# Performance work log

Measured on AMD Instinct MI355X. Metric: run time of the kernel, lower is better.

## Reference

```python
import jax, jax.numpy as jnp
import numpy as np

B, T, C = 256, 2048, 39   # batch, time, nb_filters
NB = 8                     # number of dilation levels (2**0 .. 2**7)
K = 2                      # kernel size
NC = 8                     # num_classes
EPS = 1e-5                 # BatchNorm eps (eval mode)


def _causal_conv(x, w, b, d):
    """x: [B,C,T], w: [Cout,Cin,K], left-pad (K-1)*d for causality."""
    k = w.shape[-1]
    y = jax.lax.conv_general_dilated(
        x, w, window_strides=(1,), padding=[((k - 1) * d, 0)],
        rhs_dilation=(d,), dimension_numbers=('NCH', 'OIH', 'NCH'))
    return y + b[None, :, None]


def _bn(x, g, be, m, v):
    # eval-mode BatchNorm1d with running stats
    return g[None, :, None] * (x - m[None, :, None]) * jax.lax.rsqrt(v + EPS)[None, :, None] + be[None, :, None]


def _block(x, w, b, g, be, m, v, d):
    # Temporal_Aware_Block, eval mode (dropout = identity).
    # w: [2,C,C,K], b/g/be/m/v: [2,C]
    y = jax.nn.relu(_bn(_causal_conv(x, w[0], b[0], d), g[0], be[0], m[0], v[0]))
    y = jax.nn.relu(_bn(_causal_conv(y, w[1], b[1], d), g[1], be[1], m[1], v[1]))
    # causal conv preserves length, so the 1x1 residual conv branch is never taken
    return x * jax.nn.sigmoid(y)


def setup_inputs() -> dict:
    key = jax.random.key(0)
    ks = jax.random.split(key, 24)
    f = lambda k, s: jax.random.normal(k, s, dtype=jnp.float32) * 0.1
    return {
        'inputs': jax.random.normal(ks[0], (B, T, C), dtype=jnp.float32),
        'conv1x1_w': f(ks[1], (C, C, 1)),
        'conv1x1_b': f(ks[2], (C,)),
        'fw_conv_w': f(ks[3], (NB, 2, C, C, K)),
        'fw_conv_b': f(ks[4], (NB, 2, C)),
        'fw_gamma': 1.0 + f(ks[5], (NB, 2, C)),
        'fw_beta': f(ks[6], (NB, 2, C)),
        'fw_mean': f(ks[7], (NB, 2, C)),
        'fw_var': jax.random.uniform(ks[8], (NB, 2, C), dtype=jnp.float32, minval=0.5, maxval=1.5),
        'bw_conv_w': f(ks[9], (NB, 2, C, C, K)),
        'bw_conv_b': f(ks[10], (NB, 2, C)),
        'bw_gamma': 1.0 + f(ks[11], (NB, 2, C)),
        'bw_beta': f(ks[12], (NB, 2, C)),
        'bw_mean': f(ks[13], (NB, 2, C)),
        'bw_var': jax.random.uniform(ks[14], (NB, 2, C), dtype=jnp.float32, minval=0.5, maxval=1.5),
        'wl_kernel': f(ks[15], (NB, 1)),
        'cls_w': f(ks[16], (NC, C)),
        'cls_b': f(ks[17], (NC,)),
    }


def reference(inputs, conv1x1_w, conv1x1_b,
              fw_conv_w, fw_conv_b, fw_gamma, fw_beta, fw_mean, fw_var,
              bw_conv_w, bw_conv_b, bw_gamma, bw_beta, bw_mean, bw_var,
              wl_kernel, cls_w, cls_b):
    x = jnp.transpose(inputs, (0, 2, 1))           # [B,C,T]
    fwd = _causal_conv(x, conv1x1_w, conv1x1_b, 1)
    bwd = _causal_conv(x[:, :, ::-1], conv1x1_w, conv1x1_b, 1)
    skips = []
    for i in range(NB):
        d = 2 ** i
        fwd = _block(fwd, fw_conv_w[i], fw_conv_b[i], fw_gamma[i], fw_beta[i], fw_mean[i], fw_var[i], d)
        bwd = _block(bwd, bw_conv_w[i], bw_conv_b[i], bw_gamma[i], bw_beta[i], bw_mean[i], bw_var[i], d)
        skips.append(jnp.mean(fwd + bwd, axis=-1))  # [B,C]
    g = jnp.stack(skips, axis=-1)                   # [B,C,NB]
    x2 = jnp.einsum('bcn,no->bc', g, wl_kernel)     # WeightLayer matmul + squeeze
    logits = x2 @ cls_w.T + cls_b                   # [B,NC]
    return jax.nn.log_softmax(logits, axis=1)
```

## Files before the change

### kernel.cpp

```cpp
#include <hip/hip_runtime.h>
#include <math.h>

#define BATCH 256
#define TT    2048
#define CC    39
#define CP    40
#define Y1ST  44
#define NBLK  8
#define KK    2
#define NCLS  8
#define BN_EPS 1e-5f
#define TBLK  512
#define NW    8

typedef __attribute__((ext_vector_type(8))) short short8;
typedef __attribute__((ext_vector_type(4))) float floatx4;

__device__ __forceinline__ unsigned short f2b(float f) {
    union { float f; unsigned u; } v; v.f = f;
    unsigned r = v.u + 0x7FFF + ((v.u >> 16) & 1);
    return (unsigned short)(r >> 16);
}
__device__ __forceinline__ unsigned cvtpk(float lo, float hi) {
    unsigned r;
    asm("v_cvt_pk_bf16_f32 %0, %1, %2" : "=v"(r) : "v"(lo), "v"(hi));
    return r;
}
__device__ __forceinline__ float blo(unsigned u) {
    union { unsigned v; float f; } k; k.v = u << 16; return k.f;
}
__device__ __forceinline__ float bhi(unsigned u) {
    union { unsigned v; float f; } k; k.v = u & 0xffff0000u; return k.f;
}
__device__ __forceinline__ void gl_lds16(const void* g, void* l) {
    __builtin_amdgcn_global_load_lds(
        (const __attribute__((address_space(1))) unsigned int*)g,
        (__attribute__((address_space(3))) unsigned int*)l, 16, 0, 0);
}

#define WFB_PER   (2*3*3*512)
#define WFB_TOTAL (2*NBLK*WFB_PER)
#define BFB_TOTAL (2*NBLK*2*48)
#define WFF_TOTAL (3*2*512)
#define BFF_TOTAL 48
#define ZPAD_SHORTS (256 * CP)

__global__ void fold_kernel(const float* __restrict__ fw_w, const float* __restrict__ fw_b,
                            const float* __restrict__ fw_g, const float* __restrict__ fw_be,
                            const float* __restrict__ fw_m, const float* __restrict__ fw_v,
                            const float* __restrict__ bw_w, const float* __restrict__ bw_b,
                            const float* __restrict__ bw_g, const float* __restrict__ bw_be,
                            const float* __restrict__ bw_m, const float* __restrict__ bw_v,
                            const float* __restrict__ c1w, const float* __restrict__ c1b,
                            unsigned short* __restrict__ wfb, float* __restrict__ bfb,
                            unsigned short* __restrict__ wff, float* __restrict__ bff) {
    int idx = blockIdx.x * blockDim.x + threadIdx.x;
    if (idx < WFB_TOTAL) {
        int i = idx;
        int reg = i & 7;   i >>= 3;
        int lane = i & 63; i >>= 6;
        int sl = i % 3;    i /= 3;
        int ct = i % 3;    i /= 3;
        int layer = i & 1; i >>= 1;
        int blk = i & 7;   i >>= 3;
        int dir = i;
        int g = lane >> 4;
        int co = ct * 16 + (lane & 15);
        int p, ci; bool ok = true;
        if (sl < 2) {
            int kin = (g << 3) + reg;
            p = kin >> 4;
            ci = sl * 16 + (kin & 15);
        } else {
            p = g & 1;
            ci = 32 + reg;
            ok = (g < 2);
        }
        float val = 0.f;
        if (ok && co < CC && ci < CC) {
            const float* w = dir ? bw_w : fw_w;
            const float* gam = dir ? bw_g : fw_g;
            const float* var = dir ? bw_v : fw_v;
            int il = blk * 2 + layer;
            float sc = gam[il * CC + co] * rsqrtf(var[il * CC + co] + BN_EPS);
            val = w[((size_t)(il * CC + co) * CC + ci) * KK + p] * sc;
        }
        wfb[idx] = f2b(val);
        return;
    }
    idx -= WFB_TOTAL;
    if (idx < BFB_TOTAL) {
        int co = idx % 48;
        int i = idx / 48;
        int layer = i & 1; i >>= 1;
        int blk = i & 7;   i >>= 3;
        int dir = i;
        float val = 0.f;
        if (co < CC) {
            const float* b  = dir ? bw_b  : fw_b;
            const float* g  = dir ? bw_g  : fw_g;
            const float* be = dir ? bw_be : fw_be;
            const float* m  = dir ? bw_m  : fw_m;
            const float* v  = dir ? bw_v  : fw_v;
            int r = (blk * 2 + layer) * CC + co;
            float sc = g[r] * rsqrtf(v[r] + BN_EPS);
            val = (b[r] - m[r]) * sc + be[r];
        }
        bfb[idx] = val;
        return;
    }
    idx -= BFB_TOTAL;
    if (idx < WFF_TOTAL) {
        int i = idx;
        int reg = i & 7;   i >>= 3;
        int lane = i & 63; i >>= 6;
        int sl = i & 1;    i >>= 1;
        int ct = i;
        int co = ct * 16 + (lane & 15);
        int ci = sl * 32 + ((lane >> 4) << 3) + reg;
        float val = (co < CC && ci < CC) ? c1w[co * CC + ci] : 0.f;
        wff[idx] = f2b(val);
        return;
    }
    idx -= WFF_TOTAL;
    if (idx < BFF_TOTAL) {
        bff[idx] = (idx < CC) ? c1b[idx] : 0.f;
    }
}

__global__ __launch_bounds__(TBLK) void block0_mfma(
        const float* __restrict__ in,
        const unsigned short* __restrict__ wf_all, const float* __restrict__ bf_all,
        const unsigned short* __restrict__ wff, const float* __restrict__ bff,
        unsigned short* __restrict__ yg, float* __restrict__ skipPart) {
    constexpr int D = 1;
    constexpr int ROWS_X   = 272;
    constexpr int XT_SHORTS = ROWS_X * CP;
    constexpr int M1       = 17;
    constexpr int ROWS_REAL = 256 + D;
    constexpr int Y1_SHORTS = M1 * 16 * Y1ST + 8;
    constexpr int M2W      = 256 / (16 * NW);

    extern __shared__ char ldsraw[];
    unsigned short* xt = (unsigned short*)ldsraw;
    unsigned short* y1 = xt + XT_SHORTS;
    float* stash = (float*)(y1 + Y1_SHORTS);

    const int dir = blockIdx.z, b = blockIdx.y, tile = blockIdx.x;
    const int t0 = tile * 256;
    const int tid = threadIdx.x, lane = tid & 63, wave = tid >> 6;
    const int c = lane & 15, g = lane >> 4;
    const size_t cbase = (size_t)(dir * BATCH + b) * TT * CP;

    {
        unsigned* xd = (unsigned*)xt;
        const float* inb = in + (size_t)b * TT * CC;
        for (int e = tid; e < ROWS_X * 20; e += TBLK) {
            int row = e / 20, cp = e - row * 20;
            int t = t0 - 2 + row;
            unsigned val = 0u;
            if (t >= 0 && row < 258) {
                int srow = dir ? (TT - 1 - t) : t;
                const float* sp = inb + (size_t)srow * CC + cp * 2;
                float f0 = sp[0];
                float f1 = (cp < 19) ? sp[1] : 0.f;
                val = cvtpk(f0, f1);
            }
            xd[e] = val;
        }
        if (tid < 16) ((unsigned*)(xt + XT_SHORTS))[tid] = 0;
    }

    short8 FW[3][2];
    float fbs[3][4];
#pragma unroll
    for (int ct = 0; ct < 3; ++ct) {
#pragma unroll
        for (int sl = 0; sl < 2; ++sl)
            FW[ct][sl] = *(const short8*)(wff + (((ct * 2 + sl) * 64 + lane) << 3));
#pragma unroll
        for (int j = 0; j < 4; ++j) fbs[ct][j] = bff[ct * 16 + g * 4 + j];
    }
    __syncthreads();

    for (int mt = wave; mt < M1; mt += NW) {
        int row = (mt << 4) + c;
        const unsigned short* bp = xt + row * CP;
        floatx4 acc[3];
#pragma unroll
        for (int ct = 0; ct < 3; ++ct)
            acc[ct] = floatx4{fbs[ct][0], fbs[ct][1], fbs[ct][2], fbs[ct][3]};
#pragma unroll
        for (int sl = 0; sl < 2; ++sl) {
            short8 B = *(const short8*)(bp + sl * 32 + g * 8);
#pragma unroll
            for (int ct = 0; ct < 3; ++ct)
                acc[ct] = __builtin_amdgcn_mfma_f32_16x16x32_bf16(FW[ct][sl], B, acc[ct], 0, 0, 0);
        }
        unsigned short* op = xt + row * CP;
#pragma unroll
        for (int ct = 0; ct < 3; ++ct) {
            if (ct == 2 && g >= 2) continue;
            uint2 v;
            v.x = cvtpk(acc[ct][0], acc[ct][1]);
            v.y = cvtpk(acc[ct][2], acc[ct][3]);
            *(uint2*)(op + ct * 16 + g * 4) = v;
        }
    }
    __syncthreads();

    const int r01off = (g >> 1) * D;
    const int r2off  = (g & 1) * D;
    const int koff8  = (g & 1) << 3;
    const unsigned short* wf = wf_all + (size_t)(dir * NBLK + 0) * WFB_PER;
    const float* bf = bf_all + (size_t)(dir * NBLK + 0) * 96;

    short8 Wf[3][3];
    float bs[3][4];
#pragma unroll
    for (int ct = 0; ct < 3; ++ct) {
#pragma unroll
        for (int sl = 0; sl < 3; ++sl)
            Wf[ct][sl] = *(const short8*)(wf + (((ct * 3 + sl) * 64 + lane) << 3));
#pragma unroll
        for (int j = 0; j < 4; ++j) bs[ct][j] = bf[ct * 16 + g * 4 + j];
    }

    for (int mt = wave; mt < M1; mt += NW) {
        int j0 = mt << 4;
        const unsigned short* bp01 = xt + (j0 + c + r01off) * CP + koff8;
        const unsigned short* bp2  = xt + (j0 + c + r2off) * CP + 32;
        short8 B0 = *(const short8*)(bp01);
        short8 B1 = *(const short8*)(bp01 + 16);
        short8 B2 = *(const short8*)(bp2);
        floatx4 acc[3];
#pragma unroll
        for (int ct = 0; ct < 3; ++ct) {
            acc[ct] = floatx4{bs[ct][0], bs[ct][1], bs[ct][2], bs[ct][3]};
            acc[ct] = __builtin_amdgcn_mfma_f32_16x16x32_bf16(Wf[ct][0], B0, acc[ct], 0, 0, 0);
            acc[ct] = __builtin_amdgcn_mfma_f32_16x16x32_bf16(Wf[ct][1], B1, acc[ct], 0, 0, 0);
            acc[ct] = __builtin_amdgcn_mfma_f32_16x16x32_bf16(Wf[ct][2], B2, acc[ct], 0, 0, 0);
        }
        int r = j0 + c;
        bool dead = (t0 - D + r < 0) || (r >= ROWS_REAL);
        unsigned short* yp = y1 + r * Y1ST;
#pragma unroll
        for (int ct = 0; ct < 3; ++ct) {
            if (ct == 2 && g >= 2) continue;
            uint2 v;
            v.x = cvtpk(fmaxf(acc[ct][0], 0.f), fmaxf(acc[ct][1], 0.f));
            v.y = cvtpk(fmaxf(acc[ct][2], 0.f), fmaxf(acc[ct][3], 0.f));
            if (dead) { v.x = 0u; v.y = 0u; }
            *(uint2*)(yp + ct * 16 + g * 4) = v;
        }
    }
    __syncthreads();

#pragma unroll
    for (int ct = 0; ct < 3; ++ct) {
#pragma unroll
        for (int sl = 0; sl < 3; ++sl)
            Wf[ct][sl] = *(const short8*)(wf + ((((3 + ct) * 3 + sl) * 64 + lane) << 3));
#pragma unroll
        for (int j = 0; j < 4; ++j) bs[ct][j] = bf[48 + ct * 16 + g * 4 + j];
    }

    float sums[3][4];
#pragma unroll
    for (int ct = 0; ct < 3; ++ct)
#pragma unroll
        for (int j = 0; j < 4; ++j) sums[ct][j] = 0.f;

#pragma unroll
    for (int mi = 0; mi < M2W; ++mi) {
        int j0 = (((wave * M2W) + mi) << 4);
        const unsigned short* bp01 = y1 + (j0 + c + r01off) * Y1ST + koff8;
        const unsigned short* bp2  = y1 + (j0 + c + r2off) * Y1ST + 32;
        short8 B0 = *(const short8*)(bp01);
        short8 B1 = *(const short8*)(bp01 + 16);
        short8 B2 = *(const short8*)(bp2);
        floatx4 acc[3];
#pragma unroll
        for (int ct = 0; ct < 3; ++ct) {
            acc[ct] = floatx4{bs[ct][0], bs[ct][1], bs[ct][2], bs[ct][3]};
            acc[ct] = __builtin_amdgcn_mfma_f32_16x16x32_bf16(Wf[ct][0], B0, acc[ct], 0, 0, 0);
            acc[ct] = __builtin_amdgcn_mfma_f32_16x16x32_bf16(Wf[ct][1], B1, acc[ct], 0, 0, 0);
            acc[ct] = __builtin_amdgcn_mfma_f32_16x16x32_bf16(Wf[ct][2], B2, acc[ct], 0, 0, 0);
        }
        int r = j0 + c;
        const unsigned short* xrow = xt + (r + 2 * D) * CP;
        unsigned short* orow = yg + cbase + (size_t)(t0 + r) * CP;
#pragma unroll
        for (int ct = 0; ct < 3; ++ct) {
            uint2 xv = *(const uint2*)(xrow + ct * 16 + g * 4);
            float g0 = blo(xv.x) * __builtin_amdgcn_rcpf(1.f + __expf(-acc[ct][0]));
            float g1 = bhi(xv.x) * __builtin_amdgcn_rcpf(1.f + __expf(-acc[ct][1]));
            float g2 = blo(xv.y) * __builtin_amdgcn_rcpf(1.f + __expf(-acc[ct][2]));
            float g3 = bhi(xv.y) * __builtin_amdgcn_rcpf(1.f + __expf(-acc[ct][3]));
            sums[ct][0] += g0; sums[ct][1] += g1;
            sums[ct][2] += g2; sums[ct][3] += g3;
            if (!(ct == 2 && g >= 2)) {
                uint2 v;
                v.x = cvtpk(g0, g1);
                v.y = cvtpk(g2, g3);
                *(uint2*)(orow + ct * 16 + g * 4) = v;
            }
        }
    }
#pragma unroll
    for (int ct = 0; ct < 3; ++ct)
#pragma unroll
        for (int j = 0; j < 4; ++j) {
            float v = sums[ct][j];
            v += __shfl_xor(v, 1, 64);
            v += __shfl_xor(v, 2, 64);
            v += __shfl_xor(v, 4, 64);
            v += __shfl_xor(v, 8, 64);
            sums[ct][j] = v;
        }
    if (c == 0) {
#pragma unroll
        for (int ct = 0; ct < 3; ++ct)
#pragma unroll
            for (int j = 0; j < 4; ++j)
                stash[wave * 48 + ct * 16 + g * 4 + j] = sums[ct][j];
    }
    __syncthreads();
    if (tid < CC) {
        float s = 0.f;
#pragma unroll
        for (int w = 0; w < NW; ++w) s += stash[w * 48 + tid];
        skipPart[(((size_t)(0 * 2 + dir) * BATCH + b) * CC + tid) * 16 + tile] = s;
    }
}

template <int D, int TtC>
__global__ __launch_bounds__(TBLK) void block_mfma(const unsigned short* __restrict__ xg,
                                                   unsigned short* __restrict__ yg,
                                                   const unsigned short* __restrict__ wf_all,
                                                   const float* __restrict__ bf_all,
                                                   float* __restrict__ skipPart,
                                                   const unsigned short* __restrict__ zpad,
                                                   int blk, int writeOut) {
    constexpr int NW_      = TBLK / 64;
    constexpr int ROWS_X   = TtC + 2 * D;
    constexpr int NCH      = ROWS_X * 5;
    constexpr int NIT      = (NCH + TBLK - 1) / TBLK;
    constexpr int XT_SHORTS = ROWS_X * CP;
    constexpr int M1       = (TtC + D + 15) / 16;
    constexpr int ROWS_REAL = TtC + D;
    constexpr int Y1_SHORTS = M1 * 16 * Y1ST + 8;
    constexpr int M2W      = TtC / (16 * NW_);

    extern __shared__ char ldsraw[];
    unsigned short* xt = (unsigned short*)ldsraw;
    unsigned short* y1 = xt + XT_SHORTS;
    float* stash = (float*)(y1 + Y1_SHORTS);

    const int dir = blockIdx.z, b = blockIdx.y, tile = blockIdx.x;
    const int t0 = tile * TtC;
    const int tid = threadIdx.x, lane = tid & 63, wave = tid >> 6;
    const int c = lane & 15, g = lane >> 4;

    const size_t cbase = (size_t)(dir * BATCH + b) * TT * CP;
    const unsigned short* wf = wf_all + (size_t)(dir * NBLK + blk) * WFB_PER;
    const float* bf = bf_all + (size_t)(dir * NBLK + blk) * 96;

    {
        const unsigned short* gx = xg + cbase;
#pragma unroll
        for (int it = 0; it < NIT; ++it) {
            int chunk = it * TBLK + wave * 64 + lane;
            if (chunk < NCH) {
                unsigned row = (unsigned)chunk / 5u;
                int sub = chunk - (int)row * 5;
                int t = t0 - 2 * D + (int)row;
                const unsigned short* src = (t >= 0)
                    ? (gx + (size_t)t * CP + sub * 8)
                    : (zpad + (row * CP + sub * 8));
                gl_lds16(src, xt + (size_t)(it * TBLK + wave * 64) * 8);
            }
        }
    }

    short8 Wf[3][3];
#pragma unroll
    for (int ct = 0; ct < 3; ++ct)
#pragma unroll
        for (int sl = 0; sl < 3; ++sl)
            Wf[ct][sl] = *(const short8*)(wf + ((((0 * 3 + ct) * 3 + sl) * 64 + lane) << 3));
    float bs[3][4];
#pragma unroll
    for (int ct = 0; ct < 3; ++ct)
#pragma unroll
        for (int j = 0; j < 4; ++j) bs[ct][j] = bf[ct * 16 + g * 4 + j];

    __syncthreads();

    const int r01off = (g >> 1) * D;
    const int r2off  = (g & 1) * D;
    const int koff8  = (g & 1) << 3;

    for (int mt = wave; mt < M1; mt += NW_) {
        int j0 = mt << 4;
        const unsigned short* bp01 = xt + (j0 + c + r01off) * CP + koff8;
        const unsigned short* bp2  = xt + (j0 + c + r2off) * CP + 32;
        short8 B0 = *(const short8*)(bp01);
        short8 B1 = *(const short8*)(bp01 + 16);
        short8 B2 = *(const short8*)(bp2);
        floatx4 acc[3];
#pragma unroll
        for (int ct = 0; ct < 3; ++ct) {
            acc[ct] = floatx4{bs[ct][0], bs[ct][1], bs[ct][2], bs[ct][3]};
            acc[ct] = __builtin_amdgcn_mfma_f32_16x16x32_bf16(Wf[ct][0], B0, acc[ct], 0, 0, 0);
            acc[ct] = __builtin_amdgcn_mfma_f32_16x16x32_bf16(Wf[ct][1], B1, acc[ct], 0, 0, 0);
            acc[ct] = __builtin_amdgcn_mfma_f32_16x16x32_bf16(Wf[ct][2], B2, acc[ct], 0, 0, 0);
        }
        int r = j0 + c;
        bool dead = (t0 - D + r < 0) || (r >= ROWS_REAL);
        unsigned short* yp = y1 + r * Y1ST;
#pragma unroll
        for (int ct = 0; ct < 3; ++ct) {
            if (ct == 2 && g >= 2) continue;
            uint2 v;
            v.x = cvtpk(fmaxf(acc[ct][0], 0.f), fmaxf(acc[ct][1], 0.f));
            v.y = cvtpk(fmaxf(acc[ct][2], 0.f), fmaxf(acc[ct][3], 0.f));
            if (dead) { v.x = 0u; v.y = 0u; }
            *(uint2*)(yp + ct * 16 + g * 4) = v;
        }
    }
    __syncthreads();

#pragma unroll
    for (int ct = 0; ct < 3; ++ct)
#pragma unroll
        for (int sl = 0; sl < 3; ++sl)
            Wf[ct][sl] = *(const short8*)(wf + ((((1 * 3 + ct) * 3 + sl) * 64 + lane) << 3));
#pragma unroll
    for (int ct = 0; ct < 3; ++ct)
#pragma unroll
        for (int j = 0; j < 4; ++j) bs[ct][j] = bf[48 + ct * 16 + g * 4 + j];

    float sums[3][4];
#pragma unroll
    for (int ct = 0; ct < 3; ++ct)
#pragma unroll
        for (int j = 0; j < 4; ++j) sums[ct][j] = 0.f;

#pragma unroll
    for (int mi = 0; mi < M2W; ++mi) {
        int j0 = (wave * M2W + mi) << 4;
        const unsigned short* bp01 = y1 + (j0 + c + r01off) * Y1ST + koff8;
        const unsigned short* bp2  = y1 + (j0 + c + r2off) * Y1ST + 32;
        short8 B0 = *(const short8*)(bp01);
        short8 B1 = *(const short8*)(bp01 + 16);
        short8 B2 = *(const short8*)(bp2);
        floatx4 acc[3];
#pragma unroll
        for (int ct = 0; ct < 3; ++ct) {
            acc[ct] = floatx4{bs[ct][0], bs[ct][1], bs[ct][2], bs[ct][3]};
            acc[ct] = __builtin_amdgcn_mfma_f32_16x16x32_bf16(Wf[ct][0], B0, acc[ct], 0, 0, 0);
            acc[ct] = __builtin_amdgcn_mfma_f32_16x16x32_bf16(Wf[ct][1], B1, acc[ct], 0, 0, 0);
            acc[ct] = __builtin_amdgcn_mfma_f32_16x16x32_bf16(Wf[ct][2], B2, acc[ct], 0, 0, 0);
        }
        int r = j0 + c;
        const unsigned short* xrow = xt + (r + 2 * D) * CP;
        unsigned short* orow = yg + cbase + (size_t)(t0 + r) * CP;
#pragma unroll
        for (int ct = 0; ct < 3; ++ct) {
            uint2 xv = *(const uint2*)(xrow + ct * 16 + g * 4);
            float g0 = blo(xv.x) * __builtin_amdgcn_rcpf(1.f + __expf(-acc[ct][0]));
            float g1 = bhi(xv.x) * __builtin_amdgcn_rcpf(1.f + __expf(-acc[ct][1]));
            float g2 = blo(xv.y) * __builtin_amdgcn_rcpf(1.f + __expf(-acc[ct][2]));
            float g3 = bhi(xv.y) * __builtin_amdgcn_rcpf(1.f + __expf(-acc[ct][3]));
            sums[ct][0] += g0; sums[ct][1] += g1;
            sums[ct][2] += g2; sums[ct][3] += g3;
            if (writeOut && !(ct == 2 && g >= 2)) {
                uint2 v;
                v.x = cvtpk(g0, g1);
                v.y = cvtpk(g2, g3);
                *(uint2*)(orow + ct * 16 + g * 4) = v;
            }
        }
    }
#pragma unroll
    for (int ct = 0; ct < 3; ++ct)
#pragma unroll
        for (int j = 0; j < 4; ++j) {
            float v = sums[ct][j];
            v += __shfl_xor(v, 1, 64);
            v += __shfl_xor(v, 2, 64);
            v += __shfl_xor(v, 4, 64);
            v += __shfl_xor(v, 8, 64);
            sums[ct][j] = v;
        }
    if (c == 0) {
#pragma unroll
        for (int ct = 0; ct < 3; ++ct)
#pragma unroll
            for (int j = 0; j < 4; ++j)
                stash[wave * 48 + ct * 16 + g * 4 + j] = sums[ct][j];
    }
    __syncthreads();
    if (tid < CC) {
        float s = 0.f;
#pragma unroll
        for (int w = 0; w < NW_; ++w) s += stash[w * 48 + tid];
        skipPart[(((size_t)(blk * 2 + dir) * BATCH + b) * CC + tid) * 16 + tile] = s;
    }
}

static inline size_t lds_bytes_for(int D, int Tt) {
    int rows_x = Tt + 2 * D;
    int xt_shorts = rows_x * CP;
    int m1 = (Tt + D + 15) / 16;
    int y1_shorts = m1 * 16 * Y1ST + 8;
    return (size_t)(xt_shorts + y1_shorts) * 2 + (TBLK / 64) * 48 * 4;
}

__global__ __launch_bounds__(64) void tail_kernel(const float* __restrict__ skipPart,
                                                  const float* __restrict__ wl,
                                                  const float* __restrict__ cw,
                                                  const float* __restrict__ cb,
                                                  float* __restrict__ out) {
    __shared__ float xs[CC];
    int b = blockIdx.x;
    int cth = threadIdx.x;
    if (cth < CC) {
        float x2 = 0.f;
        for (int i = 0; i < NBLK; ++i) {
            float wli = wl[i] * (1.0f / TT);
            for (int dirn = 0; dirn < 2; ++dirn) {
                const float* sp = skipPart + (((size_t)(i * 2 + dirn) * BATCH + b) * CC + cth) * 16;
                float s = 0.f;
#pragma unroll
                for (int tl = 0; tl < 8; ++tl) s += sp[tl];
                x2 = fmaf(s, wli, x2);
            }
        }
        xs[cth] = x2;
    }
    __syncthreads();
    if (threadIdx.x == 0) {
        float lg[NCLS];
        float mx = -1e30f;
        for (int o = 0; o < NCLS; ++o) {
            float a = cb[o];
#pragma unroll
            for (int cc2 = 0; cc2 < CC; ++cc2) a = fmaf(cw[o * CC + cc2], xs[cc2], a);
            lg[o] = a;
            mx = fmaxf(mx, a);
        }
        float se = 0.f;
        for (int o = 0; o < NCLS; ++o) se += expf(lg[o] - mx);
        float lse = logf(se) + mx;
        for (int o = 0; o < NCLS; ++o) out[b * NCLS + o] = lg[o] - lse;
    }
}

extern "C" void kernel_launch(void* const* d_in, const int* in_sizes, int n_in,
                              void* d_out, int out_size, void* d_ws, size_t ws_size,
                              hipStream_t stream) {
    const float* inputs = (const float*)d_in[0];
    const float* c1w    = (const float*)d_in[1];
    const float* c1b    = (const float*)d_in[2];
    const float* fw_w   = (const float*)d_in[3];
    const float* fw_b   = (const float*)d_in[4];
    const float* fw_g   = (const float*)d_in[5];
    const float* fw_be  = (const float*)d_in[6];
    const float* fw_m   = (const float*)d_in[7];
    const float* fw_v   = (const float*)d_in[8];
    const float* bw_w   = (const float*)d_in[9];
    const float* bw_b   = (const float*)d_in[10];
    const float* bw_g   = (const float*)d_in[11];
    const float* bw_be  = (const float*)d_in[12];
    const float* bw_m   = (const float*)d_in[13];
    const float* bw_v   = (const float*)d_in[14];
    const float* wl     = (const float*)d_in[15];
    const float* clsw   = (const float*)d_in[16];
    const float* clsb   = (const float*)d_in[17];

    const size_t bufsz = (size_t)2 * BATCH * TT * CP;
    unsigned short* buf0 = (unsigned short*)d_ws;
    unsigned short* buf1 = buf0 + bufsz;
    float* skip = (float*)(buf1 + bufsz);
    const size_t skipsz = (size_t)NBLK * 2 * BATCH * CC * 16;
    unsigned short* wfb = (unsigned short*)(skip + skipsz);
    float* bfb = (float*)(wfb + WFB_TOTAL);
    unsigned short* wff = (unsigned short*)(bfb + BFB_TOTAL);
    float* bff = (float*)(wff + WFF_TOTAL);
    unsigned short* zpad = (unsigned short*)(bff + BFF_TOTAL);

    hipMemsetAsync(zpad, 0, ZPAD_SHORTS * sizeof(unsigned short), stream);

    {
        int tot = WFB_TOTAL + BFB_TOTAL + WFF_TOTAL + BFF_TOTAL;
        fold_kernel<<<(tot + 255) / 256, 256, 0, stream>>>(
            fw_w, fw_b, fw_g, fw_be, fw_m, fw_v,
            bw_w, bw_b, bw_g, bw_be, bw_m, bw_v, c1w, c1b,
            wfb, bfb, wff, bff);
    }

    {
        size_t lds0 = (size_t)(272 * CP + 17 * 16 * Y1ST + 8) * 2 + (TBLK / 64) * 48 * 4 + 64;
        block0_mfma<<<dim3(TT / 256, BATCH, 2), TBLK, lds0, stream>>>(
            inputs, wfb, bfb, wff, bff, buf0, skip);
    }

    unsigned short* cur = buf0;
    unsigned short* nxt = buf1;
#define LAUNCH_BLOCK(DD)                                                             \
    block_mfma<DD, 256><<<dim3(TT / 256, BATCH, 2), TBLK, lds_bytes_for(DD, 256),    \
                          stream>>>(cur, nxt, wfb, bfb, skip, zpad, i,               \
                                    (i < NBLK - 1) ? 1 : 0)
    for (int i = 1; i < NBLK; ++i) {
        switch (i) {
            case 1: LAUNCH_BLOCK(2); break;
            case 2: LAUNCH_BLOCK(4); break;
            case 3: LAUNCH_BLOCK(8); break;
            case 4: LAUNCH_BLOCK(16); break;
            case 5: LAUNCH_BLOCK(32); break;
            case 6: LAUNCH_BLOCK(64); break;
            case 7: LAUNCH_BLOCK(128); break;
        }
        unsigned short* tmp = cur; cur = nxt; nxt = tmp;
    }
#undef LAUNCH_BLOCK

    tail_kernel<<<BATCH, 64, 0, stream>>>(skip, wl, clsw, clsb, (float*)d_out);
}
```

Baseline: 558.3 us.

## Fuse pairs of low-dilation temporal blocks into one kernel with halo recompute

Adds a pair_mfma kernel that runs two consecutive dilated blocks (levels 1-2 and 3-4) in one launch. The first block's output for the tile plus the halo the second block needs is kept in LDS, so the intermediate activation never goes through global memory. Fused launches use 128-step tiles, so there are now 16 skip partials per tile; the tail sums all 16 and the skip buffer is zeroed. The cost is recomputing halo rows and more LDS per block.

```diff
diff --git a/kernel.cpp b/kernel.cpp
--- a/kernel.cpp
+++ b/kernel.cpp
@@ -334,6 +334,315 @@
     }
 }
 
+template <int DA, int DB, int LA, int TtC>
+__global__ __launch_bounds__(TBLK) void pair_mfma(
+        const unsigned short* __restrict__ xg, unsigned short* __restrict__ yg,
+        const unsigned short* __restrict__ wf_all, const float* __restrict__ bf_all,
+        float* __restrict__ skipPart, const unsigned short* __restrict__ zpad) {
+    constexpr int HX  = 2 * DB + 2 * DA;
+    constexpr int HYA = 2 * DB + DA;
+    constexpr int RXR = TtC + HX;
+    constexpr int RYA = TtC + HYA;
+    constexpr int M1A = (RYA + 15) / 16;
+    constexpr int RXA = M1A * 16 + DA;
+    constexpr int RYB = TtC + DB;
+    constexpr int M1B = (RYB + 15) / 16;
+    constexpr int RAR = TtC + 2 * DB;
+    constexpr int RAA = ((M1B * 16 + DB + 15) / 16) * 16;
+    constexpr int M2A = RAA / 16;
+    constexpr int M2B = TtC / (16 * NW);
+    constexpr int XSH  = RXA * CP;
+    constexpr int Y1SH = M1A * 16 * Y1ST + 8;
+    constexpr int ASH  = RAA * CP;
+    constexpr int NCHA = RXA * 5;
+    constexpr int NIT  = (NCHA + TBLK - 1) / TBLK;
+    constexpr int NTIL = TT / TtC;
+
+    extern __shared__ char ldsraw[];
+    unsigned short* X  = (unsigned short*)ldsraw;
+    unsigned short* Y1 = X + XSH;
+    unsigned short* AO = Y1 + Y1SH;
+    float* stash = (float*)(AO + ASH);
+
+    const int dir = blockIdx.z, b = blockIdx.y, tile = blockIdx.x;
+    const int t0 = tile * TtC;
+    const int tid = threadIdx.x, lane = tid & 63, wave = tid >> 6;
+    const int c = lane & 15, g = lane >> 4;
+    const int koff8 = (g & 1) << 3;
+    const int oa01 = (g >> 1) * DA, oa2 = (g & 1) * DA;
+    const int ob01 = (g >> 1) * DB, ob2 = (g & 1) * DB;
+
+    const size_t cbase = (size_t)(dir * BATCH + b) * TT * CP;
+    const unsigned short* wfa = wf_all + (size_t)(dir * NBLK + LA) * WFB_PER;
+    const float* bfa = bf_all + (size_t)(dir * NBLK + LA) * 96;
+    const unsigned short* wfb2 = wf_all + (size_t)(dir * NBLK + LA + 1) * WFB_PER;
+    const float* bfb2 = bf_all + (size_t)(dir * NBLK + LA + 1) * 96;
+
+    {
+        const unsigned short* gx = xg + cbase;
+#pragma unroll
+        for (int it = 0; it < NIT; ++it) {
+            int chunk = it * TBLK + wave * 64 + lane;
+            if (chunk < NCHA) {
+                unsigned row = (unsigned)chunk / 5u;
+                int sub = chunk - (int)row * 5;
+                int t = t0 - HX + (int)row;
+                const unsigned short* src = (t >= 0 && (int)row < RXR)
+                    ? (gx + (size_t)t * CP + sub * 8)
+                    : (zpad + ((row & 255u) * CP + sub * 8));
+                gl_lds16(src, X + (size_t)(it * TBLK + wave * 64) * 8);
+            }
+        }
+    }
+
+    short8 Wf[3][3];
+    float bs[3][4];
+#pragma unroll
+    for (int ct = 0; ct < 3; ++ct) {
+#pragma unroll
+        for (int sl = 0; sl < 3; ++sl)
+            Wf[ct][sl] = *(const short8*)(wfa + (((ct * 3 + sl) * 64 + lane) << 3));
+#pragma unroll
+        for (int j = 0; j < 4; ++j) bs[ct][j] = bfa[ct * 16 + g * 4 + j];
+    }
+    __syncthreads();
+
+    for (int mt = wave; mt < M1A; mt += NW) {
+        int j0 = mt << 4;
+        const unsigned short* bp01 = X + (j0 + c + oa01) * CP + koff8;
+        const unsigned short* bp2  = X + (j0 + c + oa2) * CP + 32;
+        short8 B0 = *(const short8*)(bp01);
+        short8 B1 = *(const short8*)(bp01 + 16);
+        short8 B2 = *(const short8*)(bp2);
+        floatx4 acc[3];
+#pragma unroll
+        for (int ct = 0; ct < 3; ++ct) {
+            acc[ct] = floatx4{bs[ct][0], bs[ct][1], bs[ct][2], bs[ct][3]};
+            acc[ct] = __builtin_amdgcn_mfma_f32_16x16x32_bf16(Wf[ct][0], B0, acc[ct], 0, 0, 0);
+            acc[ct] = __builtin_amdgcn_mfma_f32_16x16x32_bf16(Wf[ct][1], B1, acc[ct], 0, 0, 0);
+            acc[ct] = __builtin_amdgcn_mfma_f32_16x16x32_bf16(Wf[ct][2], B2, acc[ct], 0, 0, 0);
+        }
+        int r = j0 + c;
+        bool dead = (t0 - HYA + r < 0) || (r >= RYA);
+        unsigned short* yp = Y1 + r * Y1ST;
+#pragma unroll
+        for (int ct = 0; ct < 3; ++ct) {
+            if (ct == 2 && g >= 2) continue;
+            uint2 v;
+            v.x = cvtpk(fmaxf(acc[ct][0], 0.f), fmaxf(acc[ct][1], 0.f));
+            v.y = cvtpk(fmaxf(acc[ct][2], 0.f), fmaxf(acc[ct][3], 0.f));
+            if (dead) { v.x = 0u; v.y = 0u; }
+            *(uint2*)(yp + ct * 16 + g * 4) = v;
+        }
+    }
+    __syncthreads();
+
+#pragma unroll
+    for (int ct = 0; ct < 3; ++ct) {
+#pragma unroll
+        for (int sl = 0; sl < 3; ++sl)
+            Wf[ct][sl] = *(const short8*)(wfa + ((((3 + ct) * 3 + sl) * 64 + lane) << 3));
+#pragma unroll
+        for (int j = 0; j < 4; ++j) bs[ct][j] = bfa[48 + ct * 16 + g * 4 + j];
+    }
+
+    float sums[3][4];
+#pragma unroll
+    for (int ct = 0; ct < 3; ++ct)
+#pragma unroll
+        for (int j = 0; j < 4; ++j) sums[ct][j] = 0.f;
+
+    for (int mt = wave; mt < M2A; mt += NW) {
+        int j0 = mt << 4;
+        const unsigned short* bp01 = Y1 + (j0 + c + oa01) * Y1ST + koff8;
+        const unsigned short* bp2  = Y1 + (j0 + c + oa2) * Y1ST + 32;
+        short8 B0 = *(const short8*)(bp01);
+        short8 B1 = *(const short8*)(bp01 + 16);
+        short8 B2 = *(const short8*)(bp2);
+        floatx4 acc[3];
+#pragma unroll
+        for (int ct = 0; ct < 3; ++ct) {
+            acc[ct] = floatx4{bs[ct][0], bs[ct][1], bs[ct][2], bs[ct][3]};
+            acc[ct] = __builtin_amdgcn_mfma_f32_16x16x32_bf16(Wf[ct][0], B0, acc[ct], 0, 0, 0);
+            acc[ct] = __builtin_amdgcn_mfma_f32_16x16x32_bf16(Wf[ct][1], B1, acc[ct], 0, 0, 0);
+            acc[ct] = __builtin_amdgcn_mfma_f32_16x16x32_bf16(Wf[ct][2], B2, acc[ct], 0, 0, 0);
+        }
+        int ra = j0 + c;
+        bool adead = (ra >= RAR);
+        bool inskip = (ra >= 2 * DB) && (ra < 2 * DB + TtC);
+        const unsigned short* xrow = X + (ra + 2 * DA) * CP;
+        unsigned short* arow = AO + ra * CP;
+#pragma unroll
+        for (int ct = 0; ct < 3; ++ct) {
+            if (ct == 2 && g >= 2) continue;
+            uint2 ov;
+            if (adead) {
+                ov.x = 0u; ov.y = 0u;
+            } else {
+                uint2 xv = *(const uint2*)(xrow + ct * 16 + g * 4);
+                float g0 = blo(xv.x) * __builtin_amdgcn_rcpf(1.f + __expf(-acc[ct][0]));
+                float g1 = bhi(xv.x) * __builtin_amdgcn_rcpf(1.f + __expf(-acc[ct][1]));
+                float g2 = blo(xv.y) * __builtin_amdgcn_rcpf(1.f + __expf(-acc[ct][2]));
+                float g3 = bhi(xv.y) * __builtin_amdgcn_rcpf(1.f + __expf(-acc[ct][3]));
+                if (inskip) {
+                    sums[ct][0] += g0; sums[ct][1] += g1;
+                    sums[ct][2] += g2; sums[ct][3] += g3;
+                }
+                ov.x = cvtpk(g0, g1);
+                ov.y = cvtpk(g2, g3);
+            }
+            *(uint2*)(arow + ct * 16 + g * 4) = ov;
+        }
+    }
+#pragma unroll
+    for (int ct = 0; ct < 3; ++ct)
+#pragma unroll
+        for (int j = 0; j < 4; ++j) {
+            float v = sums[ct][j];
+            v += __shfl_xor(v, 1, 64);
+            v += __shfl_xor(v, 2, 64);
+            v += __shfl_xor(v, 4, 64);
+            v += __shfl_xor(v, 8, 64);
+            sums[ct][j] = v;
+        }
+    if (c == 0) {
+#pragma unroll
+        for (int ct = 0; ct < 3; ++ct)
+#pragma unroll
+            for (int j = 0; j < 4; ++j)
+                stash[wave * 48 + ct * 16 + g * 4 + j] = sums[ct][j];
+    }
+    __syncthreads();
+    if (tid < CC) {
+        float s = 0.f;
+#pragma unroll
+        for (int w = 0; w < NW; ++w) s += stash[w * 48 + tid];
+        skipPart[(((size_t)(LA * 2 + dir) * BATCH + b) * CC + tid) * 16 + tile] = s;
+    }
+
+#pragma unroll
+    for (int ct = 0; ct < 3; ++ct) {
+#pragma unroll
+        for (int sl = 0; sl < 3; ++sl)
+            Wf[ct][sl] = *(const short8*)(wfb2 + (((ct * 3 + sl) * 64 + lane) << 3));
+#pragma unroll
+        for (int j = 0; j < 4; ++j) bs[ct][j] = bfb2[ct * 16 + g * 4 + j];
+    }
+    for (int mt = wave; mt < M1B; mt += NW) {
+        int j0 = mt << 4;
+        const unsigned short* bp01 = AO + (j0 + c + ob01) * CP + koff8;
+        const unsigned short* bp2  = AO + (j0 + c + ob2) * CP + 32;
+        short8 B0 = *(const short8*)(bp01);
+        short8 B1 = *(const short8*)(bp01 + 16);
+        short8 B2 = *(const short8*)(bp2);
+        floatx4 acc[3];
+#pragma unroll
+        for (int ct = 0; ct < 3; ++ct) {
+            acc[ct] = floatx4{bs[ct][0], bs[ct][1], bs[ct][2], bs[ct][3]};
+            acc[ct] = __builtin_amdgcn_mfma_f32_16x16x32_bf16(Wf[ct][0], B0, acc[ct], 0, 0, 0);
+            acc[ct] = __builtin_amdgcn_mfma_f32_16x16x32_bf16(Wf[ct][1], B1, acc[ct], 0, 0, 0);
+            acc[ct] = __builtin_amdgcn_mfma_f32_16x16x32_bf16(Wf[ct][2], B2, acc[ct], 0, 0, 0);
+        }
+        int r = j0 + c;
+        bool dead = (t0 - DB + r < 0) || (r >= RYB);
+        unsigned short* yp = Y1 + r * Y1ST;
+#pragma unroll
+        for (int ct = 0; ct < 3; ++ct) {
+            if (ct == 2 && g >= 2) continue;
+            uint2 v;
+            v.x = cvtpk(fmaxf(acc[ct][0], 0.f), fmaxf(acc[ct][1], 0.f));
+            v.y = cvtpk(fmaxf(acc[ct][2], 0.f), fmaxf(acc[ct][3], 0.f));
+            if (dead) { v.x = 0u; v.y = 0u; }
+            *(uint2*)(yp + ct * 16 + g * 4) = v;
+        }
+    }
+    __syncthreads();
+
+#pragma unroll
+    for (int ct = 0; ct < 3; ++ct) {
+#pragma unroll
+        for (int sl = 0; sl < 3; ++sl)
+            Wf[ct][sl] = *(const short8*)(wfb2 + ((((3 + ct) * 3 + sl) * 64 + lane) << 3));
+#pragma unroll
+        for (int j = 0; j < 4; ++j) bs[ct][j] = bfb2[48 + ct * 16 + g * 4 + j];
+    }
+#pragma unroll
+    for (int ct = 0; ct < 3; ++ct)
+#pragma unroll
+        for (int j = 0; j < 4; ++j) sums[ct][j] = 0.f;
+
+#pragma unroll
+    for (int mi = 0; mi < M2B; ++mi) {
+        int j0 = (wave * M2B + mi) << 4;
+        const unsigned short* bp01 = Y1 + (j0 + c + ob01) * Y1ST + koff8;
+        const unsigned short* bp2  = Y1 + (j0 + c + ob2) * Y1ST + 32;
+        short8 B0 = *(const short8*)(bp01);
+        short8 B1 = *(const short8*)(bp01 + 16);
+        short8 B2 = *(const short8*)(bp2);
+        floatx4 acc[3];
+#pragma unroll
+        for (int ct = 0; ct < 3; ++ct) {
+            acc[ct] = floatx4{bs[ct][0], bs[ct][1], bs[ct][2], bs[ct][3]};
+            acc[ct] = __builtin_amdgcn_mfma_f32_16x16x32_bf16(Wf[ct][0], B0, acc[ct], 0, 0, 0);
+            acc[ct] = __builtin_amdgcn_mfma_f32_16x16x32_bf16(Wf[ct][1], B1, acc[ct], 0, 0, 0);
+            acc[ct] = __builtin_amdgcn_mfma_f32_16x16x32_bf16(Wf[ct][2], B2, acc[ct], 0, 0, 0);
+        }
+        int rb = j0 + c;
+        const unsigned short* arow = AO + (rb + 2 * DB) * CP;
+        unsigned short* orow = yg + cbase + (size_t)(t0 + rb) * CP;
+#pragma unroll
+        for (int ct = 0; ct < 3; ++ct) {
+            uint2 xv = *(const uint2*)(arow + ct * 16 + g * 4);
+            float g0 = blo(xv.x) * __builtin_amdgcn_rcpf(1.f + __expf(-acc[ct][0]));
+            float g1 = bhi(xv.x) * __builtin_amdgcn_rcpf(1.f + __expf(-acc[ct][1]));
+            float g2 = blo(xv.y) * __builtin_amdgcn_rcpf(1.f + __expf(-acc[ct][2]));
+            float g3 = bhi(xv.y) * __builtin_amdgcn_rcpf(1.f + __expf(-acc[ct][3]));
+            sums[ct][0] += g0; sums[ct][1] += g1;
+            sums[ct][2] += g2; sums[ct][3] += g3;
+            if (!(ct == 2 && g >= 2)) {
+                uint2 v;
+                v.x = cvtpk(g0, g1);
+                v.y = cvtpk(g2, g3);
+                *(uint2*)(orow + ct * 16 + g * 4) = v;
+            }
+        }
+    }
+#pragma unroll
+    for (int ct = 0; ct < 3; ++ct)
+#pragma unroll
+        for (int j = 0; j < 4; ++j) {
+            float v = sums[ct][j];
+            v += __shfl_xor(v, 1, 64);
+            v += __shfl_xor(v, 2, 64);
+            v += __shfl_xor(v, 4, 64);
+            v += __shfl_xor(v, 8, 64);
+            sums[ct][j] = v;
+        }
+    if (c == 0) {
+#pragma unroll
+        for (int ct = 0; ct < 3; ++ct)
+#pragma unroll
+            for (int j = 0; j < 4; ++j)
+                stash[wave * 48 + ct * 16 + g * 4 + j] = sums[ct][j];
+    }
+    __syncthreads();
+    if (tid < CC) {
+        float s = 0.f;
+#pragma unroll
+        for (int w = 0; w < NW; ++w) s += stash[w * 48 + tid];
+        skipPart[(((size_t)((LA + 1) * 2 + dir) * BATCH + b) * CC + tid) * 16 + tile] = s;
+    }
+}
+
+static inline size_t pair_lds(int DA, int DB, int T) {
+    int HYA = 2 * DB + DA;
+    int M1A = (T + HYA + 15) / 16;
+    int RXA = M1A * 16 + DA;
+    int M1B = (T + DB + 15) / 16;
+    int RAA = ((M1B * 16 + DB + 15) / 16) * 16;
+    return (size_t)(RXA * CP + M1A * 16 * Y1ST + 8 + RAA * CP) * 2 + NW * 48 * 4;
+}
+
 template <int D, int TtC>
 __global__ __launch_bounds__(TBLK) void block_mfma(const unsigned short* __restrict__ xg,
                                                    unsigned short* __restrict__ yg,
@@ -534,7 +843,7 @@
                 const float* sp = skipPart + (((size_t)(i * 2 + dirn) * BATCH + b) * CC + cth) * 16;
                 float s = 0.f;
 #pragma unroll
-                for (int tl = 0; tl < 8; ++tl) s += sp[tl];
+                for (int tl = 0; tl < 16; ++tl) s += sp[tl];
                 x2 = fmaf(s, wli, x2);
             }
         }
@@ -592,6 +901,7 @@
     unsigned short* zpad = (unsigned short*)(bff + BFF_TOTAL);
 
     hipMemsetAsync(zpad, 0, ZPAD_SHORTS * sizeof(unsigned short), stream);
+    hipMemsetAsync(skip, 0, skipsz * sizeof(float), stream);
 
     {
         int tot = WFB_TOTAL + BFB_TOTAL + WFF_TOTAL + BFF_TOTAL;
@@ -607,25 +917,17 @@
             inputs, wfb, bfb, wff, bff, buf0, skip);
     }
 
-    unsigned short* cur = buf0;
-    unsigned short* nxt = buf1;
-#define LAUNCH_BLOCK(DD)                                                             \
-    block_mfma<DD, 256><<<dim3(TT / 256, BATCH, 2), TBLK, lds_bytes_for(DD, 256),    \
-                          stream>>>(cur, nxt, wfb, bfb, skip, zpad, i,               \
-                                    (i < NBLK - 1) ? 1 : 0)
-    for (int i = 1; i < NBLK; ++i) {
-        switch (i) {
-            case 1: LAUNCH_BLOCK(2); break;
-            case 2: LAUNCH_BLOCK(4); break;
-            case 3: LAUNCH_BLOCK(8); break;
-            case 4: LAUNCH_BLOCK(16); break;
-            case 5: LAUNCH_BLOCK(32); break;
-            case 6: LAUNCH_BLOCK(64); break;
-            case 7: LAUNCH_BLOCK(128); break;
-        }
-        unsigned short* tmp = cur; cur = nxt; nxt = tmp;
-    }
-#undef LAUNCH_BLOCK
+    pair_mfma<2, 4, 1, 128><<<dim3(TT / 128, BATCH, 2), TBLK, pair_lds(2, 4, 128), stream>>>(
+        buf0, buf1, wfb, bfb, skip, zpad);
+    pair_mfma<8, 16, 3, 128><<<dim3(TT / 128, BATCH, 2), TBLK, pair_lds(8, 16, 128), stream>>>(
+        buf1, buf0, wfb, bfb, skip, zpad);
+
+    block_mfma<32, 256><<<dim3(TT / 256, BATCH, 2), TBLK, lds_bytes_for(32, 256), stream>>>(
+        buf0, buf1, wfb, bfb, skip, zpad, 5, 1);
+    block_mfma<64, 256><<<dim3(TT / 256, BATCH, 2), TBLK, lds_bytes_for(64, 256), stream>>>(
+        buf1, buf0, wfb, bfb, skip, zpad, 6, 1);
+    block_mfma<128, 256><<<dim3(TT / 256, BATCH, 2), TBLK, lds_bytes_for(128, 256), stream>>>(
+        buf0, buf1, wfb, bfb, skip, zpad, 7, 0);
 
     tail_kernel<<<BATCH, 64, 0, stream>>>(skip, wl, clsw, clsb, (float*)d_out);
 }
```

Result: slower. 667.9 us (+19.6%).

## Process two time tiles per block with prefetched LDS double buffer for small dilations

Applied to the files above, without the earlier changes.

Adds a block2_mfma kernel for dilations 2–16. Each workgroup issues async global-to-LDS loads for two consecutive 256-step time tiles up front, then computes the first tile while the second tile's load is still in flight. This halves the grid for those levels and overlaps load latency with MFMA compute, at the cost of roughly double the LDS per block, which may reduce occupancy. Skip partial sums now use 16 slots, the skip buffer is zeroed with a memset, and the tail kernel sums all 16 slots.

```diff
diff --git a/kernel.cpp b/kernel.cpp
--- a/kernel.cpp
+++ b/kernel.cpp
@@ -334,6 +334,229 @@
     }
 }
 
+template <int D, int M1, int ROWS_REAL>
+__device__ __forceinline__ void conv1_tile(
+        const unsigned short* __restrict__ xt, unsigned short* __restrict__ y1,
+        const unsigned short* __restrict__ wf, const float* __restrict__ bf,
+        int t0, int wave, int lane) {
+    const int c = lane & 15, g = lane >> 4;
+    const int koff8 = (g & 1) << 3;
+    const int r01off = (g >> 1) * D;
+    const int r2off  = (g & 1) * D;
+    short8 Wf[3][3]; float bs[3][4];
+#pragma unroll
+    for (int ct = 0; ct < 3; ++ct) {
+#pragma unroll
+        for (int sl = 0; sl < 3; ++sl)
+            Wf[ct][sl] = *(const short8*)(wf + (((ct * 3 + sl) * 64 + lane) << 3));
+#pragma unroll
+        for (int j = 0; j < 4; ++j) bs[ct][j] = bf[ct * 16 + g * 4 + j];
+    }
+    for (int mt = wave; mt < M1; mt += NW) {
+        int j0 = mt << 4;
+        const unsigned short* bp01 = xt + (j0 + c + r01off) * CP + koff8;
+        const unsigned short* bp2  = xt + (j0 + c + r2off) * CP + 32;
+        short8 B0 = *(const short8*)(bp01);
+        short8 B1 = *(const short8*)(bp01 + 16);
+        short8 B2 = *(const short8*)(bp2);
+        floatx4 acc[3];
+#pragma unroll
+        for (int ct = 0; ct < 3; ++ct) {
+            acc[ct] = floatx4{bs[ct][0], bs[ct][1], bs[ct][2], bs[ct][3]};
+            acc[ct] = __builtin_amdgcn_mfma_f32_16x16x32_bf16(Wf[ct][0], B0, acc[ct], 0, 0, 0);
+            acc[ct] = __builtin_amdgcn_mfma_f32_16x16x32_bf16(Wf[ct][1], B1, acc[ct], 0, 0, 0);
+            acc[ct] = __builtin_amdgcn_mfma_f32_16x16x32_bf16(Wf[ct][2], B2, acc[ct], 0, 0, 0);
+        }
+        int r = j0 + c;
+        bool dead = (t0 - D + r < 0) || (r >= ROWS_REAL);
+        unsigned short* yp = y1 + r * 40;
+#pragma unroll
+        for (int ct = 0; ct < 3; ++ct) {
+            if (ct == 2 && g >= 2) continue;
+            uint2 v;
+            v.x = cvtpk(fmaxf(acc[ct][0], 0.f), fmaxf(acc[ct][1], 0.f));
+            v.y = cvtpk(fmaxf(acc[ct][2], 0.f), fmaxf(acc[ct][3], 0.f));
+            if (dead) { v.x = 0u; v.y = 0u; }
+            *(uint2*)(yp + ct * 16 + g * 4) = v;
+        }
+    }
+}
+
+template <int D, int M2W>
+__device__ __forceinline__ void conv2_tile(
+        const unsigned short* __restrict__ xt, const unsigned short* __restrict__ y1,
+        const unsigned short* __restrict__ wf, const float* __restrict__ bf,
+        unsigned short* __restrict__ ygb, int t0, int wave, int lane,
+        int writeOut, float (&sums)[3][4]) {
+    const int c = lane & 15, g = lane >> 4;
+    const int koff8 = (g & 1) << 3;
+    const int r01off = (g >> 1) * D;
+    const int r2off  = (g & 1) * D;
+    short8 Wf[3][3]; float bs[3][4];
+#pragma unroll
+    for (int ct = 0; ct < 3; ++ct) {
+#pragma unroll
+        for (int sl = 0; sl < 3; ++sl)
+            Wf[ct][sl] = *(const short8*)(wf + ((((3 + ct) * 3 + sl) * 64 + lane) << 3));
+#pragma unroll
+        for (int j = 0; j < 4; ++j) bs[ct][j] = bf[48 + ct * 16 + g * 4 + j];
+    }
+#pragma unroll
+    for (int mi = 0; mi < M2W; ++mi) {
+        int j0 = (wave * M2W + mi) << 4;
+        const unsigned short* bp01 = y1 + (j0 + c + r01off) * 40 + koff8;
+        const unsigned short* bp2  = y1 + (j0 + c + r2off) * 40 + 32;
+        short8 B0 = *(const short8*)(bp01);
+        short8 B1 = *(const short8*)(bp01 + 16);
+        short8 B2 = *(const short8*)(bp2);
+        floatx4 acc[3];
+#pragma unroll
+        for (int ct = 0; ct < 3; ++ct) {
+            acc[ct] = floatx4{bs[ct][0], bs[ct][1], bs[ct][2], bs[ct][3]};
+            acc[ct] = __builtin_amdgcn_mfma_f32_16x16x32_bf16(Wf[ct][0], B0, acc[ct], 0, 0, 0);
+            acc[ct] = __builtin_amdgcn_mfma_f32_16x16x32_bf16(Wf[ct][1], B1, acc[ct], 0, 0, 0);
+            acc[ct] = __builtin_amdgcn_mfma_f32_16x16x32_bf16(Wf[ct][2], B2, acc[ct], 0, 0, 0);
+        }
+        int r = j0 + c;
+        const unsigned short* xrow = xt + (r + 2 * D) * CP;
+        unsigned short* orow = ygb + (size_t)(t0 + r) * CP;
+#pragma unroll
+        for (int ct = 0; ct < 3; ++ct) {
+            uint2 xv = *(const uint2*)(xrow + ct * 16 + g * 4);
+            float g0 = blo(xv.x) * __builtin_amdgcn_rcpf(1.f + __expf(-acc[ct][0]));
+            float g1 = bhi(xv.x) * __builtin_amdgcn_rcpf(1.f + __expf(-acc[ct][1]));
+            float g2 = blo(xv.y) * __builtin_amdgcn_rcpf(1.f + __expf(-acc[ct][2]));
+            float g3 = bhi(xv.y) * __builtin_amdgcn_rcpf(1.f + __expf(-acc[ct][3]));
+            sums[ct][0] += g0; sums[ct][1] += g1;
+            sums[ct][2] += g2; sums[ct][3] += g3;
+            if (writeOut && !(ct == 2 && g >= 2)) {
+                uint2 v;
+                v.x = cvtpk(g0, g1);
+                v.y = cvtpk(g2, g3);
+                *(uint2*)(orow + ct * 16 + g * 4) = v;
+            }
+        }
+    }
+}
+
+template <int D>
+__global__ __launch_bounds__(TBLK) void block2_mfma(
+        const unsigned short* __restrict__ xg, unsigned short* __restrict__ yg,
+        const unsigned short* __restrict__ wf_all, const float* __restrict__ bf_all,
+        float* __restrict__ skipPart, const unsigned short* __restrict__ zpad,
+        int blk, int writeOut) {
+    constexpr int T = 256;
+    constexpr int ROWS_X = T + 2 * D;
+    constexpr int NCH = ROWS_X * 5;
+    constexpr int NIT = (NCH + TBLK - 1) / TBLK;
+    static_assert(NIT == 3, "vmcnt literal assumes NIT==3 (D<=16)");
+    constexpr int XT_CH = NIT * TBLK;
+    constexpr int XT_SHORTS = XT_CH * 8;
+    constexpr int M1 = (T + D + 15) / 16;
+    constexpr int ROWS_REAL = T + D;
+    constexpr int Y1_SHORTS = M1 * 16 * 40 + 8;
+    constexpr int M2W = T / (16 * NW);
+
+    extern __shared__ char ldsraw[];
+    unsigned short* xtA = (unsigned short*)ldsraw;
+    unsigned short* xtB = xtA + XT_SHORTS;
+    unsigned short* y1  = xtB + XT_SHORTS;
+    float* stash = (float*)(y1 + Y1_SHORTS);
+
+    const int dir = blockIdx.z, b = blockIdx.y, pairid = blockIdx.x;
+    const int t0a = pairid * 2 * T, t0b = t0a + T;
+    const int tid = threadIdx.x, lane = tid & 63, wave = tid >> 6;
+    const int c = lane & 15, g = lane >> 4;
+
+    const size_t cbase = (size_t)(dir * BATCH + b) * TT * CP;
+    const unsigned short* wf = wf_all + (size_t)(dir * NBLK + blk) * WFB_PER;
+    const float* bf = bf_all + (size_t)(dir * NBLK + blk) * 96;
+    const unsigned short* gx = xg + cbase;
+    unsigned short* ygb = yg + cbase;
+
+#pragma unroll
+    for (int half = 0; half < 2; ++half) {
+        unsigned short* xt = half ? xtB : xtA;
+        const int t0 = half ? t0b : t0a;
+#pragma unroll
+        for (int it = 0; it < NIT; ++it) {
+            int chunk = it * TBLK + wave * 64 + lane;
+            unsigned row = (unsigned)chunk / 5u;
+            int sub = chunk - (int)row * 5;
+            int t = t0 - 2 * D + (int)row;
+            const unsigned short* src = (chunk < NCH && t >= 0)
+                ? (gx + (size_t)t * CP + sub * 8)
+                : (zpad + ((row & 255u) * CP + sub * 8));
+            gl_lds16(src, xt + (size_t)(it * TBLK + wave * 64) * 8);
+        }
+    }
+    asm volatile("s_waitcnt vmcnt(3)" ::: "memory");
+    __builtin_amdgcn_sched_barrier(0);
+    __builtin_amdgcn_s_barrier();
+
+    float sums2[2][3][4];
+#pragma unroll
+    for (int h = 0; h < 2; ++h)
+#pragma unroll
+        for (int ct = 0; ct < 3; ++ct)
+#pragma unroll
+            for (int j = 0; j < 4; ++j) sums2[h][ct][j] = 0.f;
+
+    conv1_tile<D, M1, ROWS_REAL>(xtA, y1, wf, bf, t0a, wave, lane);
+    __syncthreads();
+    conv2_tile<D, M2W>(xtA, y1, wf, bf, ygb, t0a, wave, lane, writeOut, sums2[0]);
+    asm volatile("s_waitcnt lgkmcnt(0)" ::: "memory");
+    __builtin_amdgcn_sched_barrier(0);
+    __builtin_amdgcn_s_barrier();
+
+    conv1_tile<D, M1, ROWS_REAL>(xtB, y1, wf, bf, t0b, wave, lane);
+    __syncthreads();
+    conv2_tile<D, M2W>(xtB, y1, wf, bf, ygb, t0b, wave, lane, writeOut, sums2[1]);
+
+#pragma unroll
+    for (int h = 0; h < 2; ++h)
+#pragma unroll
+        for (int ct = 0; ct < 3; ++ct)
+#pragma unroll
+            for (int j = 0; j < 4; ++j) {
+                float v = sums2[h][ct][j];
+                v += __shfl_xor(v, 1, 64);
+                v += __shfl_xor(v, 2, 64);
+                v += __shfl_xor(v, 4, 64);
+                v += __shfl_xor(v, 8, 64);
+                sums2[h][ct][j] = v;
+            }
+    if (c == 0) {
+#pragma unroll
+        for (int h = 0; h < 2; ++h)
+#pragma unroll
+            for (int ct = 0; ct < 3; ++ct)
+#pragma unroll
+                for (int j = 0; j < 4; ++j)
+                    stash[(h * NW + wave) * 48 + ct * 16 + g * 4 + j] = sums2[h][ct][j];
+    }
+    __syncthreads();
+    if (tid < CC) {
+#pragma unroll
+        for (int h = 0; h < 2; ++h) {
+            float s = 0.f;
+#pragma unroll
+            for (int w = 0; w < NW; ++w) s += stash[(h * NW + w) * 48 + tid];
+            skipPart[(((size_t)(blk * 2 + dir) * BATCH + b) * CC + tid) * 16
+                     + pairid * 2 + h] = s;
+        }
+    }
+}
+
+static inline size_t lds2_bytes(int D) {
+    int rows_x = 256 + 2 * D;
+    int nit = (rows_x * 5 + TBLK - 1) / TBLK;
+    int xt_shorts = nit * TBLK * 8;
+    int m1 = (256 + D + 15) / 16;
+    int y1_shorts = m1 * 16 * 40 + 8;
+    return (size_t)(2 * xt_shorts + y1_shorts) * 2 + 2 * NW * 48 * 4;
+}
+
 template <int D, int TtC>
 __global__ __launch_bounds__(TBLK) void block_mfma(const unsigned short* __restrict__ xg,
                                                    unsigned short* __restrict__ yg,
@@ -534,7 +757,7 @@
                 const float* sp = skipPart + (((size_t)(i * 2 + dirn) * BATCH + b) * CC + cth) * 16;
                 float s = 0.f;
 #pragma unroll
-                for (int tl = 0; tl < 8; ++tl) s += sp[tl];
+                for (int tl = 0; tl < 16; ++tl) s += sp[tl];
                 x2 = fmaf(s, wli, x2);
             }
         }
@@ -592,6 +815,7 @@
     unsigned short* zpad = (unsigned short*)(bff + BFF_TOTAL);
 
     hipMemsetAsync(zpad, 0, ZPAD_SHORTS * sizeof(unsigned short), stream);
+    hipMemsetAsync(skip, 0, skipsz * sizeof(float), stream);
 
     {
         int tot = WFB_TOTAL + BFB_TOTAL + WFF_TOTAL + BFF_TOTAL;
@@ -607,25 +831,21 @@
             inputs, wfb, bfb, wff, bff, buf0, skip);
     }
 
-    unsigned short* cur = buf0;
-    unsigned short* nxt = buf1;
-#define LAUNCH_BLOCK(DD)                                                             \
-    block_mfma<DD, 256><<<dim3(TT / 256, BATCH, 2), TBLK, lds_bytes_for(DD, 256),    \
-                          stream>>>(cur, nxt, wfb, bfb, skip, zpad, i,               \
-                                    (i < NBLK - 1) ? 1 : 0)
-    for (int i = 1; i < NBLK; ++i) {
-        switch (i) {
-            case 1: LAUNCH_BLOCK(2); break;
-            case 2: LAUNCH_BLOCK(4); break;
-            case 3: LAUNCH_BLOCK(8); break;
-            case 4: LAUNCH_BLOCK(16); break;
-            case 5: LAUNCH_BLOCK(32); break;
-            case 6: LAUNCH_BLOCK(64); break;
-            case 7: LAUNCH_BLOCK(128); break;
-        }
-        unsigned short* tmp = cur; cur = nxt; nxt = tmp;
-    }
-#undef LAUNCH_BLOCK
+    block2_mfma<2><<<dim3(TT / 512, BATCH, 2), TBLK, lds2_bytes(2), stream>>>(
+        buf0, buf1, wfb, bfb, skip, zpad, 1, 1);
+    block2_mfma<4><<<dim3(TT / 512, BATCH, 2), TBLK, lds2_bytes(4), stream>>>(
+        buf1, buf0, wfb, bfb, skip, zpad, 2, 1);
+    block2_mfma<8><<<dim3(TT / 512, BATCH, 2), TBLK, lds2_bytes(8), stream>>>(
+        buf0, buf1, wfb, bfb, skip, zpad, 3, 1);
+    block2_mfma<16><<<dim3(TT / 512, BATCH, 2), TBLK, lds2_bytes(16), stream>>>(
+        buf1, buf0, wfb, bfb, skip, zpad, 4, 1);
+
+    block_mfma<32, 256><<<dim3(TT / 256, BATCH, 2), TBLK, lds_bytes_for(32, 256), stream>>>(
+        buf0, buf1, wfb, bfb, skip, zpad, 5, 1);
+    block_mfma<64, 256><<<dim3(TT / 256, BATCH, 2), TBLK, lds_bytes_for(64, 256), stream>>>(
+        buf1, buf0, wfb, bfb, skip, zpad, 6, 1);
+    block_mfma<128, 256><<<dim3(TT / 256, BATCH, 2), TBLK, lds_bytes_for(128, 256), stream>>>(
+        buf0, buf1, wfb, bfb, skip, zpad, 7, 0);
 
     tail_kernel<<<BATCH, 64, 0, stream>>>(skip, wl, clsw, clsb, (float*)d_out);
 }
```

Result: slower. 621.9 us (+11.4%).
